# Kernel tuning notes

Hardware: AMD Instinct MI355X
Metric: run time of the kernel (lower is better)

Reference implementation:

```python
import jax, jax.numpy as jnp
import numpy as np

WET_MIX = 0.3
FEEDBACK = 0.4
ROOM_SIZE = 0.5
NUM_REFL = 8
NUM_HEADS = 4

# Delay kernel table: int(delay) in {0,1,2,>=3} -> kernel_size {identity,3,5,7}.
# A k-tap kernel with padding k//2 == the same kernel zero-padded to 7 taps with padding 3.
def _gauss7(ks):
    g = np.exp(-np.linspace(-2.0, 2.0, ks) ** 2)
    g = g / g.sum()
    out = np.zeros(7, np.float32)
    s = (7 - ks) // 2
    out[s:s + ks] = g
    return out
_delta = np.zeros(7, np.float32); _delta[3] = 1.0
K_TABLE = jnp.asarray(np.stack([_delta, _gauss7(3), _gauss7(5), _gauss7(7)]))  # [4,7]


def _conv2d(x, w, b, pad):
    y = jax.lax.conv_general_dilated(x, w, (1, 1), [(pad, pad), (pad, pad)],
                                     dimension_numbers=('NCHW', 'OIHW', 'NCHW'))
    return y + b[None, :, None, None]


def _delay_line(x, kern7):
    # vertical depthwise Gaussian blur, same for every (batch, channel) plane
    b, c, h, w = x.shape
    k = kern7.reshape(1, 1, 7, 1)
    y = jax.lax.conv_general_dilated(x.reshape(b * c, 1, h, w), k, (1, 1), [(3, 3), (0, 0)],
                                     dimension_numbers=('NCHW', 'OIHW', 'NCHW'))
    return y.reshape(b, c, h, w)


def _forward(x, refl_w, refl_d, sc_w, sc_b, fb_w, fb_b, d1_w, d1_b, d2_w, d2_b,
             in_proj_w, in_proj_b, out_proj_w, out_proj_b, oc_w, oc_b):
    B, C, H, W = x.shape
    scaled = refl_d * ROOM_SIZE
    kidx = jnp.clip(jnp.floor(scaled).astype(jnp.int32), 0, 3)  # int(delay) detaches grad, as in torch

    wet = jnp.zeros_like(x)
    fb_buf = x * 0.1
    spatial = _conv2d(x, sc_w, sc_b, 1)  # [B,2C,H,W]

    for i in range(NUM_REFL):
        refl = _delay_line(fb_buf, K_TABLE[kidx[i]])
        refl = _conv2d(refl, fb_w, fb_b, 1)
        damp = jax.nn.sigmoid(_conv2d(jax.nn.silu(_conv2d(refl, d1_w, d1_b, 0)), d2_w, d2_b, 0))
        refl = refl * damp
        weight = jax.nn.sigmoid(refl_w[i]) * (0.8 ** i)
        wet = wet + refl * weight
        fb_buf = fb_buf + refl * (FEEDBACK * 0.1)

    # MultiheadAttention over L = H*W tokens, embed_dim=C=4, 4 heads (head_dim=1)
    L = H * W
    hd = C // NUM_HEADS
    wet_flat = wet.reshape(B, C, L).transpose(0, 2, 1)           # [B,L,C]
    qkv = wet_flat @ in_proj_w.T + in_proj_b                     # [B,L,3C]
    q, k, v = jnp.split(qkv, 3, axis=-1)
    def heads(t):
        return t.reshape(B, L, NUM_HEADS, hd).transpose(0, 2, 1, 3)  # [B,H,L,hd]
    q, k, v = heads(q), heads(k), heads(v)
    scores = jnp.einsum('bhqd,bhkd->bhqk', q, k) / np.sqrt(hd).astype(np.float32)
    attn = jax.nn.softmax(scores, axis=-1)
    o = jnp.einsum('bhqk,bhkd->bhqd', attn, v)
    o = o.transpose(0, 2, 1, 3).reshape(B, L, C) @ out_proj_w.T + out_proj_b
    wet2 = o.transpose(0, 2, 1).reshape(B, C, H, W)

    combined = jnp.concatenate([spatial, wet2], axis=1)          # [B,3C,H,W]
    processed_wet = _conv2d(combined, oc_w, oc_b, 0)
    return x * (1.0 - WET_MIX) + processed_wet * WET_MIX


def setup_inputs() -> dict:
    key = jax.random.key(0)
    ks = jax.random.split(key, 16)
    B, C, H, W = 2, 4, 64, 64
    f32 = jnp.float32
    return {
        'x': jax.random.normal(ks[0], (B, C, H, W), f32),
        'refl_w': jax.random.normal(ks[1], (8,), f32) * 0.1,
        'refl_d': jax.random.randint(ks[2], (8,), 1, 16).astype(f32),
        'sc_w': jax.random.normal(ks[3], (2 * C, C, 3, 3), f32) * 0.1,
        'sc_b': jnp.zeros((2 * C,), f32),
        'fb_w': jax.random.normal(ks[4], (C, C, 3, 3), f32) * 0.1,
        'fb_b': jnp.zeros((C,), f32),
        'd1_w': jax.random.normal(ks[5], (C // 2, C, 1, 1), f32) * 0.3,
        'd1_b': jnp.zeros((C // 2,), f32),
        'd2_w': jax.random.normal(ks[6], (C, C // 2, 1, 1), f32) * 0.3,
        'd2_b': jnp.zeros((C,), f32),
        'in_proj_w': jax.random.normal(ks[7], (3 * C, C), f32) * 0.3,
        'in_proj_b': jnp.zeros((3 * C,), f32),
        'out_proj_w': jax.random.normal(ks[8], (C, C), f32) * 0.3,
        'out_proj_b': jnp.zeros((C,), f32),
        'oc_w': jax.random.normal(ks[9], (C, 3 * C, 1, 1), f32) * 0.2,
        'oc_b': jnp.zeros((C,), f32),
    }


def reference(x, refl_w, refl_d, sc_w, sc_b, fb_w, fb_b, d1_w, d1_b, d2_w, d2_b,
              in_proj_w, in_proj_b, out_proj_w, out_proj_b, oc_w, oc_b):
    return _forward(x, refl_w, refl_d, sc_w, sc_b, fb_w, fb_b, d1_w, d1_b, d2_w, d2_b,
                    in_proj_w, in_proj_b, out_proj_w, out_proj_b, oc_w, oc_b)
```

## Files before the change

### kernel.cpp

```cpp
#include <hip/hip_runtime.h>
#include <math.h>


#define ZERO4 make_float4(0.f, 0.f, 0.f, 0.f)

__device__ __forceinline__ float sigf(float v) { return 1.0f / (1.0f + __expf(-v)); }

__device__ __forceinline__ float dppL(float v) {
    return __int_as_float(__builtin_amdgcn_mov_dpp(__float_as_int(v), 0x138, 0xf, 0xf, true));
}
__device__ __forceinline__ float dppR(float v) {
    return __int_as_float(__builtin_amdgcn_mov_dpp(__float_as_int(v), 0x130, 0xf, 0xf, true));
}
__device__ __forceinline__ float4 shL4(float4 v) {
    return make_float4(dppL(v.x), dppL(v.y), dppL(v.z), dppL(v.w));
}
__device__ __forceinline__ float4 shR4(float4 v) {
    return make_float4(dppR(v.x), dppR(v.y), dppR(v.z), dppR(v.w));
}

__device__ __forceinline__ void tap(float4& a, const float4 t, const float* wp) {
    a.x += wp[0]   * t.x + wp[9]    * t.y + wp[18]    * t.z + wp[27]    * t.w;
    a.y += wp[36]  * t.x + wp[36+9] * t.y + wp[36+18] * t.z + wp[36+27] * t.w;
    a.z += wp[72]  * t.x + wp[72+9] * t.y + wp[72+18] * t.z + wp[72+27] * t.w;
    a.w += wp[108] * t.x + wp[108+9]* t.y + wp[108+18]* t.z + wp[108+27]* t.w;
}

__global__ __launch_bounds__(1024, 1) void reverb_qkv_kernel(
    const float* __restrict__ x,
    const float* __restrict__ refl_w,
    const float* __restrict__ refl_d,
    const float* __restrict__ fb_w,
    const float* __restrict__ fb_b,
    const float* __restrict__ d1_w,
    const float* __restrict__ d1_b,
    const float* __restrict__ d2_w,
    const float* __restrict__ d2_b,
    const float* __restrict__ ipw,
    const float* __restrict__ ipb,
    float* __restrict__ Qg, float* __restrict__ Kg, float* __restrict__ Vg)
{
    __shared__ float4 P [18 * 64];
    __shared__ float4 BL[18 * 64];
    __shared__ float4 WT[2 * 64];
    __shared__ float  GT[3][8];

    const int blk   = blockIdx.x;
    const int batch = blk >> 5;
    const int own0  = (blk & 31) << 1;
    const int LB    = own0 - 8;
    const int tid   = threadIdx.x;
    const int wy    = tid >> 6;
    const int r     = tid & 63;

    if (tid < 3) {
        const int rr = tid + 1;
        const int ks = 2 * rr + 1;
        const int s  = (7 - ks) >> 1;
        const double step = 4.0 / (double)(ks - 1);
        double g[7]; double sum = 0.0;
        for (int t = 0; t < 7; ++t) {
            if (t < ks) { double u = -2.0 + step * (double)t; g[t] = exp(-u * u); sum += g[t]; }
        }
        for (int t = 0; t < 7; ++t) GT[tid][t] = 0.0f;
        for (int t = 0; t < ks; ++t) GT[tid][s + t] = (float)(g[t] / sum);
    }

    for (int idx = tid; idx < 18 * 64; idx += 1024) {
        const int lc  = idx >> 6;
        const int row = idx & 63;
        const int gc  = LB + lc;
        float4 v = ZERO4;
        if (gc >= 0 && gc < 64) {
            const int base = batch * 16384 + row * 64 + gc;
            v.x = 0.1f * x[base];
            v.y = 0.1f * x[base + 4096];
            v.z = 0.1f * x[base + 8192];
            v.w = 0.1f * x[base + 12288];
        }
        P[idx] = v;
    }
    __syncthreads();

    double w8 = 1.0;
    for (int j = 0; j < 8; ++j) {
        int kidx = (int)floorf(refl_d[j] * 0.5f);
        kidx = kidx < 0 ? 0 : (kidx > 3 ? 3 : kidx);
        float kv[7];
        #pragma unroll
        for (int u = 0; u < 7; ++u) {
            const float dv = (u == 3) ? 1.0f : 0.0f;
            kv[u] = (kidx == 0) ? dv : GT[kidx - 1][u];
        }
        const float wgt = sigf(refl_w[j]) * (float)w8;

        for (int lc = wy; lc < 18; lc += 16) {
            const int gc = LB + lc;
            float4 b = ZERO4;
            if (gc >= 0 && gc < 64) {
                const float4 v  = P[lc * 64 + r];
                const float4 l1 = shL4(v),  l2 = shL4(l1), l3 = shL4(l2);
                const float4 r1 = shR4(v),  r2 = shR4(r1), r3 = shR4(r2);
                b.x = kv[0]*l3.x + kv[1]*l2.x + kv[2]*l1.x + kv[3]*v.x
                    + kv[4]*r1.x + kv[5]*r2.x + kv[6]*r3.x;
                b.y = kv[0]*l3.y + kv[1]*l2.y + kv[2]*l1.y + kv[3]*v.y
                    + kv[4]*r1.y + kv[5]*r2.y + kv[6]*r3.y;
                b.z = kv[0]*l3.z + kv[1]*l2.z + kv[2]*l1.z + kv[3]*v.z
                    + kv[4]*r1.z + kv[5]*r2.z + kv[6]*r3.z;
                b.w = kv[0]*l3.w + kv[1]*l2.w + kv[2]*l1.w + kv[3]*v.w
                    + kv[4]*r1.w + kv[5]*r2.w + kv[6]*r3.w;
            }
            BL[lc * 64 + r] = b;
        }
        __syncthreads();

        const int clo = max(0, own0 - (7 - j));
        const int chi = min(64, own0 + 2 + (7 - j));
        const int c   = clo + wy;
        if (wy < chi - clo) {
            const int lc = c - LB;
            const float4 bm = BL[(lc - 1) * 64 + r];
            const float4 bc = BL[lc * 64 + r];
            const float4 bp = BL[(lc + 1) * 64 + r];

            float4 acc = make_float4(fb_b[0], fb_b[1], fb_b[2], fb_b[3]);
            tap(acc, shL4(bm), fb_w + 0);  tap(acc, shL4(bc), fb_w + 1);  tap(acc, shL4(bp), fb_w + 2);
            tap(acc, bm,       fb_w + 3);  tap(acc, bc,       fb_w + 4);  tap(acc, bp,       fb_w + 5);
            tap(acc, shR4(bm), fb_w + 6);  tap(acc, shR4(bc), fb_w + 7);  tap(acc, shR4(bp), fb_w + 8);

            float4 rr = acc;
            float h0 = d1_b[0] + d1_w[0]*rr.x + d1_w[1]*rr.y + d1_w[2]*rr.z + d1_w[3]*rr.w;
            float h1 = d1_b[1] + d1_w[4]*rr.x + d1_w[5]*rr.y + d1_w[6]*rr.z + d1_w[7]*rr.w;
            h0 = h0 * sigf(h0);
            h1 = h1 * sigf(h1);
            const float d0  = sigf(d2_b[0] + d2_w[0]*h0 + d2_w[1]*h1);
            const float d1v = sigf(d2_b[1] + d2_w[2]*h0 + d2_w[3]*h1);
            const float d2v = sigf(d2_b[2] + d2_w[4]*h0 + d2_w[5]*h1);
            const float d3v = sigf(d2_b[3] + d2_w[6]*h0 + d2_w[7]*h1);
            rr.x *= d0; rr.y *= d1v; rr.z *= d2v; rr.w *= d3v;

            const float4 oldfb = P[lc * 64 + r];
            P[lc * 64 + r] = make_float4(oldfb.x + 0.04f*rr.x, oldfb.y + 0.04f*rr.y,
                                         oldfb.z + 0.04f*rr.z, oldfb.w + 0.04f*rr.w);

            if (c >= own0 && c < own0 + 2) {
                const int widx = (c - own0) * 64 + r;
                float4 wv = make_float4(wgt*rr.x, wgt*rr.y, wgt*rr.z, wgt*rr.w);
                if (j > 0) {
                    const float4 old = WT[widx];
                    wv.x += old.x; wv.y += old.y; wv.z += old.z; wv.w += old.w;
                }
                WT[widx] = wv;
            }
        }
        __syncthreads();
        w8 *= 0.8;
    }

    if (tid < 128) {
        const int row = tid & 63;
        const int oc  = tid >> 6;
        const int c   = own0 + oc;
        const float4 wv = WT[oc * 64 + row];
        #pragma unroll
        for (int h = 0; h < 4; ++h) {
            const float q = ipb[h]
                + ipw[h*4+0]*wv.x + ipw[h*4+1]*wv.y
                + ipw[h*4+2]*wv.z + ipw[h*4+3]*wv.w;
            const float k = ipb[4+h]
                + ipw[(4+h)*4+0]*wv.x + ipw[(4+h)*4+1]*wv.y
                + ipw[(4+h)*4+2]*wv.z + ipw[(4+h)*4+3]*wv.w;
            const float v = ipb[8+h]
                + ipw[(8+h)*4+0]*wv.x + ipw[(8+h)*4+1]*wv.y
                + ipw[(8+h)*4+2]*wv.z + ipw[(8+h)*4+3]*wv.w;
            const int o = (batch * 4 + h) * 4096 + row * 64 + c;
            Qg[o] = q; Kg[o] = k; Vg[o] = v;
        }
    }
}

__global__ __launch_bounds__(256) void attn_kernel(
    const float* __restrict__ Qg, const float* __restrict__ Kg,
    const float* __restrict__ Vg, float* __restrict__ OH)
{
    __shared__ float2 KV[4096];
    __shared__ float  wred[8];
    __shared__ float  partN[256], partD[256];

    const int bh  = blockIdx.x >> 6;
    const int sub = blockIdx.x & 63;
    const int tid = threadIdx.x;

    const float* Kp = Kg + bh * 4096;
    const float* Vp = Vg + bh * 4096;

    float pmax = -3.0e38f, pmin = 3.0e38f;
    for (int t = tid; t < 4096; t += 256) {
        const float kv = Kp[t];
        const float vv = Vp[t];
        KV[t] = make_float2(kv, vv);
        pmax = fmaxf(pmax, kv);
        pmin = fminf(pmin, kv);
    }
    #pragma unroll
    for (int off = 32; off > 0; off >>= 1) {
        pmax = fmaxf(pmax, __shfl_xor(pmax, off, 64));
        pmin = fminf(pmin, __shfl_xor(pmin, off, 64));
    }
    if ((tid & 63) == 0) { wred[tid >> 6] = pmax; wred[4 + (tid >> 6)] = pmin; }
    __syncthreads();
    const float kmax = fmaxf(fmaxf(wred[0], wred[1]), fmaxf(wred[2], wred[3]));
    const float kmin = fminf(fminf(wred[4], wred[5]), fminf(wred[6], wred[7]));

    const int ql = tid & 63;
    const int kh = tid >> 6;
    const int qi = sub * 64 + ql;
    const float q = Qg[bh * 4096 + qi];
    const float m = (q >= 0.0f) ? q * kmax : q * kmin;

    const float4* KV4 = (const float4*)KV;
    const int base4 = kh * 512;

    float num0 = 0.f, num1 = 0.f, den0 = 0.f, den1 = 0.f;
    for (int j = 0; j < 512; j += 4) {
        #pragma unroll
        for (int u = 0; u < 4; ++u) {
            const float4 f = KV4[base4 + j + u];
            const float e0 = __expf(__fmaf_rn(q, f.x, -m));
            const float e1 = __expf(__fmaf_rn(q, f.z, -m));
            den0 += e0;  den1 += e1;
            num0 = __fmaf_rn(e0, f.y, num0);
            num1 = __fmaf_rn(e1, f.w, num1);
        }
    }
    partN[tid] = num0 + num1;
    partD[tid] = den0 + den1;
    __syncthreads();
    if (tid < 64) {
        const float n = partN[tid] + partN[tid + 64] + partN[tid + 128] + partN[tid + 192];
        const float d = partD[tid] + partD[tid + 64] + partD[tid + 128] + partD[tid + 192];
        OH[bh * 4096 + sub * 64 + tid] = n / d;
    }
}

__global__ __launch_bounds__(128) void final_kernel(
    const float* __restrict__ x,
    const float* __restrict__ sc_w, const float* __restrict__ sc_b,
    const float* __restrict__ opw,  const float* __restrict__ opb,
    const float* __restrict__ ocw,  const float* __restrict__ ocb,
    const float* __restrict__ OH,   float* __restrict__ out)
{
    const int g   = blockIdx.x * 128 + threadIdx.x;
    const int b   = g >> 12;
    const int pix = g & 4095;
    const int y   = pix >> 6;
    const int xc  = pix & 63;

    float xin[4][3][3];
    #pragma unroll
    for (int ic = 0; ic < 4; ++ic)
        #pragma unroll
        for (int ky = 0; ky < 3; ++ky)
            #pragma unroll
            for (int kx = 0; kx < 3; ++kx) {
                const int yy = y + ky - 1, xx = xc + kx - 1;
                xin[ic][ky][kx] = (yy >= 0 && yy < 64 && xx >= 0 && xx < 64)
                                    ? x[(b * 4 + ic) * 4096 + yy * 64 + xx] : 0.f;
            }

    float sp[8];
    #pragma unroll
    for (int oc = 0; oc < 8; ++oc) {
        float a = sc_b[oc];
        #pragma unroll
        for (int ic = 0; ic < 4; ++ic)
            #pragma unroll
            for (int ky = 0; ky < 3; ++ky)
                #pragma unroll
                for (int kx = 0; kx < 3; ++kx)
                    a += sc_w[(oc * 4 + ic) * 9 + ky * 3 + kx] * xin[ic][ky][kx];
        sp[oc] = a;
    }

    float oh[4];
    #pragma unroll
    for (int h = 0; h < 4; ++h) oh[h] = OH[(b * 4 + h) * 4096 + pix];

    float w2[4];
    #pragma unroll
    for (int c = 0; c < 4; ++c)
        w2[c] = opb[c] + opw[c*4+0]*oh[0] + opw[c*4+1]*oh[1]
                       + opw[c*4+2]*oh[2] + opw[c*4+3]*oh[3];

    #pragma unroll
    for (int c = 0; c < 4; ++c) {
        float a = ocb[c];
        #pragma unroll
        for (int j = 0; j < 8; ++j) a += ocw[c * 12 + j] * sp[j];
        #pragma unroll
        for (int h = 0; h < 4; ++h) a += ocw[c * 12 + 8 + h] * w2[h];
        const int idx = (b * 4 + c) * 4096 + y * 64 + xc;
        out[idx] = 0.7f * x[idx] + 0.3f * a;
    }
}

extern "C" void kernel_launch(void* const* d_in, const int* in_sizes, int n_in,
                              void* d_out, int out_size, void* d_ws, size_t ws_size,
                              hipStream_t stream) {
    const float* x      = (const float*)d_in[0];
    const float* refl_w = (const float*)d_in[1];
    const float* refl_d = (const float*)d_in[2];
    const float* sc_w   = (const float*)d_in[3];
    const float* sc_b   = (const float*)d_in[4];
    const float* fb_w   = (const float*)d_in[5];
    const float* fb_b   = (const float*)d_in[6];
    const float* d1_w   = (const float*)d_in[7];
    const float* d1_b   = (const float*)d_in[8];
    const float* d2_w   = (const float*)d_in[9];
    const float* d2_b   = (const float*)d_in[10];
    const float* ipw    = (const float*)d_in[11];
    const float* ipb    = (const float*)d_in[12];
    const float* opw    = (const float*)d_in[13];
    const float* opb    = (const float*)d_in[14];
    const float* ocw    = (const float*)d_in[15];
    const float* ocb    = (const float*)d_in[16];
    float* out = (float*)d_out;

    float* Q  = (float*)d_ws;
    float* K  = Q + 32768;
    float* V  = K + 32768;
    float* OH = V + 32768;

    reverb_qkv_kernel<<<dim3(64), dim3(1024), 0, stream>>>(
        x, refl_w, refl_d, fb_w, fb_b, d1_w, d1_b, d2_w, d2_b, ipw, ipb,
        Q, K, V);
    attn_kernel<<<dim3(512), dim3(256), 0, stream>>>(Q, K, V, OH);
    final_kernel<<<dim3(64), dim3(128), 0, stream>>>(
        x, sc_w, sc_b, opw, opb, ocw, ocb, OH, out);
}
```

Baseline: 144.4 us.

## Read K/V directly from global with wave-uniform loads and trim blur rows

The attention kernel no longer stages K and V into shared memory. Each wave reads K/V as float4 with a wave-uniform index via readfirstlane, so the loads can become scalar or broadcast loads, and exp is computed as exp2 with prescaled q. The reverb kernel now blurs only the rows each iteration's feedback conv actually needs, instead of all 18. Each block still scans all of K for min/max, and the inner loop now depends on global or L1 bandwidth rather than LDS.

```diff
diff --git a/kernel.cpp b/kernel.cpp
--- a/kernel.cpp
+++ b/kernel.cpp
@@ -94,7 +94,13 @@
         }
         const float wgt = sigf(refl_w[j]) * (float)w8;
 
-        for (int lc = wy; lc < 18; lc += 16) {
+        const int clo = max(0, own0 - (7 - j));
+        const int chi = min(64, own0 + 2 + (7 - j));
+
+        const int lcA   = (clo - 1) - LB;
+        const int nBlur = (chi + 1) - (clo - 1);
+        for (int t = wy; t < nBlur; t += 16) {
+            const int lc = lcA + t;
             const int gc = LB + lc;
             float4 b = ZERO4;
             if (gc >= 0 && gc < 64) {
@@ -114,9 +120,7 @@
         }
         __syncthreads();
 
-        const int clo = max(0, own0 - (7 - j));
-        const int chi = min(64, own0 + 2 + (7 - j));
-        const int c   = clo + wy;
+        const int c = clo + wy;
         if (wy < chi - clo) {
             const int lc = c - LB;
             const float4 bm = BL[(lc - 1) * 64 + r];
@@ -183,9 +187,8 @@
     const float* __restrict__ Qg, const float* __restrict__ Kg,
     const float* __restrict__ Vg, float* __restrict__ OH)
 {
-    __shared__ float2 KV[4096];
-    __shared__ float  wred[8];
-    __shared__ float  partN[256], partD[256];
+    __shared__ float wred[8];
+    __shared__ float partN[256], partD[256];
 
     const int bh  = blockIdx.x >> 6;
     const int sub = blockIdx.x & 63;
@@ -196,11 +199,9 @@
 
     float pmax = -3.0e38f, pmin = 3.0e38f;
     for (int t = tid; t < 4096; t += 256) {
-        const float kv = Kp[t];
-        const float vv = Vp[t];
-        KV[t] = make_float2(kv, vv);
-        pmax = fmaxf(pmax, kv);
-        pmin = fminf(pmin, kv);
+        const float kk = Kp[t];
+        pmax = fmaxf(pmax, kk);
+        pmin = fminf(pmin, kk);
     }
     #pragma unroll
     for (int off = 32; off > 0; off >>= 1) {
@@ -213,25 +214,33 @@
     const float kmin = fminf(fminf(wred[4], wred[5]), fminf(wred[6], wred[7]));
 
     const int ql = tid & 63;
-    const int kh = tid >> 6;
+    const int kh = __builtin_amdgcn_readfirstlane(tid >> 6);
     const int qi = sub * 64 + ql;
-    const float q = Qg[bh * 4096 + qi];
-    const float m = (q >= 0.0f) ? q * kmax : q * kmin;
-
-    const float4* KV4 = (const float4*)KV;
-    const int base4 = kh * 512;
+
+    const float L2E = 1.4426950408889634f;
+    const float q  = Qg[bh * 4096 + qi];
+    const float q2 = q * L2E;
+    const float nm2 = -(((q >= 0.0f) ? q * kmax : q * kmin) * L2E);
+
+    const float4* K4 = (const float4*)Kp;
+    const float4* V4 = (const float4*)Vp;
+    const int base = kh * 256;
 
     float num0 = 0.f, num1 = 0.f, den0 = 0.f, den1 = 0.f;
-    for (int j = 0; j < 512; j += 4) {
-        #pragma unroll
-        for (int u = 0; u < 4; ++u) {
-            const float4 f = KV4[base4 + j + u];
-            const float e0 = __expf(__fmaf_rn(q, f.x, -m));
-            const float e1 = __expf(__fmaf_rn(q, f.z, -m));
-            den0 += e0;  den1 += e1;
-            num0 = __fmaf_rn(e0, f.y, num0);
-            num1 = __fmaf_rn(e1, f.w, num1);
-        }
+    for (int j = 0; j < 256; j += 2) {
+        const float4 ka = K4[base + j];
+        const float4 kb = K4[base + j + 1];
+        const float4 va = V4[base + j];
+        const float4 vb = V4[base + j + 1];
+        float e;
+        e = exp2f(__fmaf_rn(q2, ka.x, nm2)); den0 += e; num0 = __fmaf_rn(e, va.x, num0);
+        e = exp2f(__fmaf_rn(q2, ka.y, nm2)); den1 += e; num1 = __fmaf_rn(e, va.y, num1);
+        e = exp2f(__fmaf_rn(q2, ka.z, nm2)); den0 += e; num0 = __fmaf_rn(e, va.z, num0);
+        e = exp2f(__fmaf_rn(q2, ka.w, nm2)); den1 += e; num1 = __fmaf_rn(e, va.w, num1);
+        e = exp2f(__fmaf_rn(q2, kb.x, nm2)); den0 += e; num0 = __fmaf_rn(e, vb.x, num0);
+        e = exp2f(__fmaf_rn(q2, kb.y, nm2)); den1 += e; num1 = __fmaf_rn(e, vb.y, num1);
+        e = exp2f(__fmaf_rn(q2, kb.z, nm2)); den0 += e; num0 = __fmaf_rn(e, vb.z, num0);
+        e = exp2f(__fmaf_rn(q2, kb.w, nm2)); den1 += e; num1 = __fmaf_rn(e, vb.w, num1);
     }
     partN[tid] = num0 + num1;
     partD[tid] = den0 + den1;
```

Measured after the change: 161.4 us. 1.12x slower.
